# Optimization experiments

Hardware: AMD Instinct MI355X
Metric: run time of the kernel (lower is better)

The kernel has to match this reference:

```python
import jax, jax.numpy as jnp
import numpy as np

N = 1024      # num_motifs == num_nodes (edge index i*N+j must fit in N*N table)
H = 128       # hidden_dim


def setup_inputs() -> dict:
    key = jax.random.key(0)
    k1, k2, k3, k4, k5, k6, k7 = jax.random.split(key, 7)
    s = 1.0 / np.sqrt(H)  # torch default init scale for Embedding-like/GRUCell params
    node_features = jax.random.normal(k1, (N, H), dtype=jnp.float32)
    adjacency_matrix = jax.random.randint(k2, (N, N), 0, 2, dtype=jnp.int32)
    edge_table = jax.random.normal(k3, (N * N, H), dtype=jnp.float32)  # nn.Embedding weight
    w_ih = jax.random.uniform(k4, (3 * H, H), minval=-s, maxval=s, dtype=jnp.float32)
    w_hh = jax.random.uniform(k5, (3 * H, H), minval=-s, maxval=s, dtype=jnp.float32)
    b_ih = jax.random.uniform(k6, (3 * H,), minval=-s, maxval=s, dtype=jnp.float32)
    b_hh = jax.random.uniform(k7, (3 * H,), minval=-s, maxval=s, dtype=jnp.float32)
    return {"node_features": node_features, "adjacency_matrix": adjacency_matrix,
            "edge_table": edge_table, "w_ih": w_ih, "w_hh": w_hh,
            "b_ih": b_ih, "b_hh": b_hh}


def reference(node_features, adjacency_matrix, edge_table, w_ih, w_hh, b_ih, b_hh):
    n, h = node_features.shape
    # edge embedding for edge (i, j) lives at row i*N + j -> view table as [N, N, H]
    T = edge_table.reshape(n, n, h)
    adj = adjacency_matrix.astype(node_features.dtype)
    # aggregated[i] = sum_{j : adj[i,j]=1} node_features[j] * edge_emb[i, j]
    agg = jnp.einsum('ij,jh,ijh->ih', adj, node_features, T)
    # GRUCell(input=agg, hidden=node_features), torch semantics
    gi = agg @ w_ih.T + b_ih              # [N, 3H]
    gh = node_features @ w_hh.T + b_hh    # [N, 3H]
    ir, iz, in_ = jnp.split(gi, 3, axis=-1)
    hr, hz, hn = jnp.split(gh, 3, axis=-1)
    r = jax.nn.sigmoid(ir + hr)
    z = jax.nn.sigmoid(iz + hz)
    nn_ = jnp.tanh(in_ + r * hn)
    return (1.0 - z) * nn_ + z * node_features
```

## Files before the change

### kernel.cpp

```cpp
#include <hip/hip_runtime.h>
#include <math.h>

#define N_NODES 1024
#define HDIM    128

__global__ __launch_bounds__(256) void motif_gru_kernel(
    const float* __restrict__ nf,
    const int*   __restrict__ adj,
    const float* __restrict__ T,
    const float* __restrict__ w_ih,
    const float* __restrict__ w_hh,
    const float* __restrict__ b_ih,
    const float* __restrict__ b_hh,
    float*       __restrict__ out)
{
    const int i   = blockIdx.x;
    const int tid = threadIdx.x;

    __shared__ int   s_list[N_NODES];
    __shared__ int   s_cnt;
    __shared__ float s_red[8][HDIM];
    __shared__ float s_agg[HDIM];
    __shared__ float s_nfi[HDIM];
    __shared__ float s_gi[3 * HDIM];
    __shared__ float s_gh[3 * HDIM];

    if (tid == 0) s_cnt = 0;
    __syncthreads();

    const int* adj_row = adj + (size_t)i * N_NODES;
    #pragma unroll
    for (int jj = 0; jj < N_NODES / 256; ++jj) {
        int j = tid + jj * 256;
        if (adj_row[j] != 0) {
            int pos = atomicAdd(&s_cnt, 1);
            s_list[pos] = j;
        }
    }
    if (tid < HDIM) s_nfi[tid] = nf[(size_t)i * HDIM + tid];
    __syncthreads();
    const int cnt = s_cnt;

    const int g    = tid >> 5;
    const int lane = tid & 31;

    const float4* Tv  = reinterpret_cast<const float4*>(T);
    const float4* nfv = reinterpret_cast<const float4*>(nf);
    const size_t rowbase = (size_t)i * N_NODES;

    float4 acc = make_float4(0.f, 0.f, 0.f, 0.f);

    int base = 0;
    for (; base + 16 <= cnt; base += 16) {
        int j0 = s_list[base + g];
        int j1 = s_list[base + 8 + g];
        float4 t0 = Tv[(rowbase + (size_t)j0) * 32 + lane];
        float4 n0 = nfv[(size_t)j0 * 32 + lane];
        float4 t1 = Tv[(rowbase + (size_t)j1) * 32 + lane];
        float4 n1 = nfv[(size_t)j1 * 32 + lane];
        acc.x += t0.x * n0.x; acc.y += t0.y * n0.y;
        acc.z += t0.z * n0.z; acc.w += t0.w * n0.w;
        acc.x += t1.x * n1.x; acc.y += t1.y * n1.y;
        acc.z += t1.z * n1.z; acc.w += t1.w * n1.w;
    }
    for (; base + 8 <= cnt; base += 8) {
        int j0 = s_list[base + g];
        float4 t0 = Tv[(rowbase + (size_t)j0) * 32 + lane];
        float4 n0 = nfv[(size_t)j0 * 32 + lane];
        acc.x += t0.x * n0.x; acc.y += t0.y * n0.y;
        acc.z += t0.z * n0.z; acc.w += t0.w * n0.w;
    }
    if (base + g < cnt) {
        int j0 = s_list[base + g];
        float4 t0 = Tv[(rowbase + (size_t)j0) * 32 + lane];
        float4 n0 = nfv[(size_t)j0 * 32 + lane];
        acc.x += t0.x * n0.x; acc.y += t0.y * n0.y;
        acc.z += t0.z * n0.z; acc.w += t0.w * n0.w;
    }

    reinterpret_cast<float4*>(&s_red[g][0])[lane] = acc;
    __syncthreads();

    if (tid < HDIM) {
        float s = 0.f;
        #pragma unroll
        for (int gg = 0; gg < 8; ++gg) s += s_red[gg][tid];
        s_agg[tid] = s;
    }
    __syncthreads();

    const float4* aggv = reinterpret_cast<const float4*>(s_agg);
    const float4* nfiv = reinterpret_cast<const float4*>(s_nfi);
    for (int c = tid; c < 3 * HDIM; c += 256) {
        const float4* wi = reinterpret_cast<const float4*>(w_ih + (size_t)c * HDIM);
        const float4* wh = reinterpret_cast<const float4*>(w_hh + (size_t)c * HDIM);
        float gs = 0.f, hs = 0.f;
        #pragma unroll 8
        for (int k = 0; k < HDIM / 4; ++k) {
            float4 w4 = wi[k]; float4 a4 = aggv[k];
            gs += w4.x * a4.x + w4.y * a4.y + w4.z * a4.z + w4.w * a4.w;
            float4 v4 = wh[k]; float4 n4 = nfiv[k];
            hs += v4.x * n4.x + v4.y * n4.y + v4.z * n4.z + v4.w * n4.w;
        }
        s_gi[c] = gs + b_ih[c];
        s_gh[c] = hs + b_hh[c];
    }
    __syncthreads();

    if (tid < HDIM) {
        float r  = 1.f / (1.f + expf(-(s_gi[tid] + s_gh[tid])));
        float z  = 1.f / (1.f + expf(-(s_gi[HDIM + tid] + s_gh[HDIM + tid])));
        float nn = tanhf(s_gi[2 * HDIM + tid] + r * s_gh[2 * HDIM + tid]);
        out[(size_t)i * HDIM + tid] = (1.f - z) * nn + z * s_nfi[tid];
    }
}

extern "C" void kernel_launch(void* const* d_in, const int* in_sizes, int n_in,
                              void* d_out, int out_size, void* d_ws, size_t ws_size,
                              hipStream_t stream) {
    const float* nf   = (const float*)d_in[0];
    const int*   adj  = (const int*)d_in[1];
    const float* T    = (const float*)d_in[2];
    const float* w_ih = (const float*)d_in[3];
    const float* w_hh = (const float*)d_in[4];
    const float* b_ih = (const float*)d_in[5];
    const float* b_hh = (const float*)d_in[6];
    float* out = (float*)d_out;

    motif_gru_kernel<<<dim3(N_NODES), dim3(256), 0, stream>>>(
        nf, adj, T, w_ih, w_hh, b_ih, b_hh, out);
}
```

Before: 678.1 us.

## Use prefix-sum compaction, nontemporal T loads, deeper unroll, vector GRU dots

Adjacency compaction now uses int4 loads plus a wave-level shuffle prefix scan instead of per-element shared atomics, and it produces an ordered neighbor list. The gather loop is unrolled to four edges per group with nontemporal loads for the streamed edge table, so more loads are in flight and the L2 sees less pollution. The GRU matvec keeps vector accumulators and reduces them at the end. This adds shuffle overhead, changes floating-point summation order, and uses more registers.

```diff
diff --git a/kernel.cpp b/kernel.cpp
--- a/kernel.cpp
+++ b/kernel.cpp
@@ -3,6 +3,8 @@
 
 #define N_NODES 1024
 #define HDIM    128
+
+typedef float f4 __attribute__((ext_vector_type(4)));
 
 __global__ __launch_bounds__(256) void motif_gru_kernel(
     const float* __restrict__ nf,
@@ -14,71 +16,86 @@
     const float* __restrict__ b_hh,
     float*       __restrict__ out)
 {
-    const int i   = blockIdx.x;
-    const int tid = threadIdx.x;
+    const int i    = blockIdx.x;
+    const int tid  = threadIdx.x;
+    const int wave = tid >> 6;
+    const int l64  = tid & 63;
 
     __shared__ int   s_list[N_NODES];
-    __shared__ int   s_cnt;
+    __shared__ int   s_wsum[4];
     __shared__ float s_red[8][HDIM];
     __shared__ float s_agg[HDIM];
     __shared__ float s_nfi[HDIM];
     __shared__ float s_gi[3 * HDIM];
     __shared__ float s_gh[3 * HDIM];
 
-    if (tid == 0) s_cnt = 0;
+    const int4 a = reinterpret_cast<const int4*>(adj + (size_t)i * N_NODES)[tid];
+    const int m0 = (a.x != 0), m1 = (a.y != 0), m2 = (a.z != 0), m3 = (a.w != 0);
+    unsigned c = (unsigned)(m0 + m1 + m2 + m3);
+    unsigned inc = c;
+    #pragma unroll
+    for (int d = 1; d < 64; d <<= 1) {
+        unsigned v = __shfl_up(inc, d);
+        if (l64 >= d) inc += v;
+    }
+    if (l64 == 63) s_wsum[wave] = (int)inc;
+    if (tid < HDIM) s_nfi[tid] = nf[(size_t)i * HDIM + tid];
     __syncthreads();
 
-    const int* adj_row = adj + (size_t)i * N_NODES;
+    int wbase = 0;
     #pragma unroll
-    for (int jj = 0; jj < N_NODES / 256; ++jj) {
-        int j = tid + jj * 256;
-        if (adj_row[j] != 0) {
-            int pos = atomicAdd(&s_cnt, 1);
-            s_list[pos] = j;
-        }
-    }
-    if (tid < HDIM) s_nfi[tid] = nf[(size_t)i * HDIM + tid];
+    for (int w = 0; w < 4; ++w) if (w < wave) wbase += s_wsum[w];
+    int pos = wbase + (int)(inc - c);
+    const int j4 = tid * 4;
+    if (m0) s_list[pos++] = j4;
+    if (m1) s_list[pos++] = j4 + 1;
+    if (m2) s_list[pos++] = j4 + 2;
+    if (m3) s_list[pos++] = j4 + 3;
     __syncthreads();
-    const int cnt = s_cnt;
+    const int cnt = s_wsum[0] + s_wsum[1] + s_wsum[2] + s_wsum[3];
 
     const int g    = tid >> 5;
     const int lane = tid & 31;
 
-    const float4* Tv  = reinterpret_cast<const float4*>(T);
-    const float4* nfv = reinterpret_cast<const float4*>(nf);
+    const f4* Tv  = reinterpret_cast<const f4*>(T);
+    const f4* nfv = reinterpret_cast<const f4*>(nf);
     const size_t rowbase = (size_t)i * N_NODES;
 
-    float4 acc = make_float4(0.f, 0.f, 0.f, 0.f);
+    f4 acc = {0.f, 0.f, 0.f, 0.f};
 
     int base = 0;
-    for (; base + 16 <= cnt; base += 16) {
-        int j0 = s_list[base + g];
-        int j1 = s_list[base + 8 + g];
-        float4 t0 = Tv[(rowbase + (size_t)j0) * 32 + lane];
-        float4 n0 = nfv[(size_t)j0 * 32 + lane];
-        float4 t1 = Tv[(rowbase + (size_t)j1) * 32 + lane];
-        float4 n1 = nfv[(size_t)j1 * 32 + lane];
-        acc.x += t0.x * n0.x; acc.y += t0.y * n0.y;
-        acc.z += t0.z * n0.z; acc.w += t0.w * n0.w;
-        acc.x += t1.x * n1.x; acc.y += t1.y * n1.y;
-        acc.z += t1.z * n1.z; acc.w += t1.w * n1.w;
+    for (; base + 32 <= cnt; base += 32) {
+        const int j0 = s_list[base      + g];
+        const int j1 = s_list[base +  8 + g];
+        const int j2 = s_list[base + 16 + g];
+        const int j3 = s_list[base + 24 + g];
+        f4 t0 = __builtin_nontemporal_load(&Tv[(rowbase + (size_t)j0) * 32 + lane]);
+        f4 t1 = __builtin_nontemporal_load(&Tv[(rowbase + (size_t)j1) * 32 + lane]);
+        f4 t2 = __builtin_nontemporal_load(&Tv[(rowbase + (size_t)j2) * 32 + lane]);
+        f4 t3 = __builtin_nontemporal_load(&Tv[(rowbase + (size_t)j3) * 32 + lane]);
+        f4 n0 = nfv[(size_t)j0 * 32 + lane];
+        f4 n1 = nfv[(size_t)j1 * 32 + lane];
+        f4 n2 = nfv[(size_t)j2 * 32 + lane];
+        f4 n3 = nfv[(size_t)j3 * 32 + lane];
+        acc += t0 * n0;
+        acc += t1 * n1;
+        acc += t2 * n2;
+        acc += t3 * n3;
     }
     for (; base + 8 <= cnt; base += 8) {
-        int j0 = s_list[base + g];
-        float4 t0 = Tv[(rowbase + (size_t)j0) * 32 + lane];
-        float4 n0 = nfv[(size_t)j0 * 32 + lane];
-        acc.x += t0.x * n0.x; acc.y += t0.y * n0.y;
-        acc.z += t0.z * n0.z; acc.w += t0.w * n0.w;
+        const int j0 = s_list[base + g];
+        f4 t0 = __builtin_nontemporal_load(&Tv[(rowbase + (size_t)j0) * 32 + lane]);
+        f4 n0 = nfv[(size_t)j0 * 32 + lane];
+        acc += t0 * n0;
     }
     if (base + g < cnt) {
-        int j0 = s_list[base + g];
-        float4 t0 = Tv[(rowbase + (size_t)j0) * 32 + lane];
-        float4 n0 = nfv[(size_t)j0 * 32 + lane];
-        acc.x += t0.x * n0.x; acc.y += t0.y * n0.y;
-        acc.z += t0.z * n0.z; acc.w += t0.w * n0.w;
+        const int j0 = s_list[base + g];
+        f4 t0 = __builtin_nontemporal_load(&Tv[(rowbase + (size_t)j0) * 32 + lane]);
+        f4 n0 = nfv[(size_t)j0 * 32 + lane];
+        acc += t0 * n0;
     }
 
-    reinterpret_cast<float4*>(&s_red[g][0])[lane] = acc;
+    reinterpret_cast<f4*>(&s_red[g][0])[lane] = acc;
     __syncthreads();
 
     if (tid < HDIM) {
@@ -89,21 +106,20 @@
     }
     __syncthreads();
 
-    const float4* aggv = reinterpret_cast<const float4*>(s_agg);
-    const float4* nfiv = reinterpret_cast<const float4*>(s_nfi);
-    for (int c = tid; c < 3 * HDIM; c += 256) {
-        const float4* wi = reinterpret_cast<const float4*>(w_ih + (size_t)c * HDIM);
-        const float4* wh = reinterpret_cast<const float4*>(w_hh + (size_t)c * HDIM);
-        float gs = 0.f, hs = 0.f;
+    const f4* aggv = reinterpret_cast<const f4*>(s_agg);
+    const f4* nfiv = reinterpret_cast<const f4*>(s_nfi);
+    for (int ci = tid; ci < 3 * HDIM; ci += 256) {
+        const f4* wi = reinterpret_cast<const f4*>(w_ih + (size_t)ci * HDIM);
+        const f4* wh = reinterpret_cast<const f4*>(w_hh + (size_t)ci * HDIM);
+        f4 gs4 = {0.f, 0.f, 0.f, 0.f};
+        f4 hs4 = {0.f, 0.f, 0.f, 0.f};
         #pragma unroll 8
         for (int k = 0; k < HDIM / 4; ++k) {
-            float4 w4 = wi[k]; float4 a4 = aggv[k];
-            gs += w4.x * a4.x + w4.y * a4.y + w4.z * a4.z + w4.w * a4.w;
-            float4 v4 = wh[k]; float4 n4 = nfiv[k];
-            hs += v4.x * n4.x + v4.y * n4.y + v4.z * n4.z + v4.w * n4.w;
+            gs4 += wi[k] * aggv[k];
+            hs4 += wh[k] * nfiv[k];
         }
-        s_gi[c] = gs + b_ih[c];
-        s_gh[c] = hs + b_hh[c];
+        s_gi[ci] = gs4.x + gs4.y + gs4.z + gs4.w + b_ih[ci];
+        s_gh[ci] = hs4.x + hs4.y + hs4.z + hs4.w + b_hh[ci];
     }
     __syncthreads();
 
```

New measurement: 682.6 us. No clear change (+0.7%).
